# Performance work log

Hardware: AMD Instinct MI355X
Metric: run time of the kernel (lower is better)

The kernel has to match this reference:

```python
import jax, jax.numpy as jnp
import numpy as np
import math

B, S, HID = 4, 2048, 1024
H, D = 16, HID // 16


def setup_inputs() -> dict:
    key = jax.random.key(0)
    ks = jax.random.split(key, 6)
    scale = 0.02
    inp = {
        "hidden_states": jax.random.normal(ks[0], (B, S, HID), dtype=jnp.float32),
        "Wq": jax.random.normal(ks[1], (HID, HID), dtype=jnp.float32) * scale,
        "bq": jnp.zeros((HID,), dtype=jnp.float32),
        "Wk1": jax.random.normal(ks[2], (HID, HID), dtype=jnp.float32) * scale,
        "bk1": jnp.zeros((HID,), dtype=jnp.float32),
        "Wk2": jax.random.normal(ks[3], (HID, HID), dtype=jnp.float32) * scale,
        "bk2": jnp.zeros((HID,), dtype=jnp.float32),
        "Wv1": jax.random.normal(ks[4], (HID, HID), dtype=jnp.float32) * scale,
        "bv1": jnp.zeros((HID,), dtype=jnp.float32),
        "Wv2": jax.random.normal(ks[5], (HID, HID), dtype=jnp.float32) * scale,
        "bv2": jnp.zeros((HID,), dtype=jnp.float32),
    }
    return inp


def _heads(x):
    # [B, S, HID] -> [B, H, S, D]
    return x.reshape(B, S, H, D).transpose(0, 2, 1, 3)


def reference(hidden_states, Wq, bq, Wk1, bk1, Wk2, bk2, Wv1, bv1, Wv2, bv2):
    # nn.Linear uses y = x @ W^T + b
    q = _heads(hidden_states @ Wq.T + bq)
    k1 = _heads(hidden_states @ Wk1.T + bk1)
    k2 = _heads(hidden_states @ Wk2.T + bk2)
    v1 = _heads(hidden_states @ Wv1.T + bv1)
    v2 = _heads(hidden_states @ Wv2.T + bv2)

    inv_sqrt_d = 1.0 / math.sqrt(D)
    scores = jnp.einsum('bhqd,bhkd->bhqk', q, k1) * inv_sqrt_d  # [B,H,S,S]
    probs = jax.nn.softmax(scores, axis=-1)
    ctx = jnp.einsum('bhqk,bhkd->bhqd', probs, v1)              # [B,H,S,D]
    ctx = jnp.einsum('bhqd,bhkd->bhqk', ctx, k2)                # [B,H,S,S]
    ctx = jnp.einsum('bhqk,bhkd->bhqd', ctx, v2)                # [B,H,S,D]
    # [B,H,S,D] -> [B,S,HID]
    return ctx.transpose(0, 2, 1, 3).reshape(B, S, HID)
```

## Files before the change

### kernel.cpp

```cpp
#include <hip/hip_runtime.h>
#include <hip/hip_bf16.h>

#define HIDD 1024
#define BATCH 4
#define SEQ 2048
#define NHEAD 16
#define HD 64
#define NW 5
#define MROWS (BATCH*SEQ)
#define NCOLS (NW*HIDD)

typedef __attribute__((ext_vector_type(8))) short bf16x8;
typedef __attribute__((ext_vector_type(4))) float f32x4;
typedef __attribute__((ext_vector_type(16))) float f32x16;
typedef __attribute__((ext_vector_type(4))) unsigned int uint4v;

__device__ __forceinline__ unsigned short f2b(float f) {
    __hip_bfloat16 h = __float2bfloat16(f);
    return __builtin_bit_cast(unsigned short, h);
}
__device__ __forceinline__ float b2f(unsigned short u) {
    __hip_bfloat16 h = __builtin_bit_cast(__hip_bfloat16, u);
    return __bfloat162float(h);
}

#if __has_builtin(__builtin_amdgcn_exp2f)
#define EXP2(x) __builtin_amdgcn_exp2f(x)
#else
#define EXP2(x) exp2f(x)
#endif

typedef __attribute__((address_space(1))) const void gvoid;
typedef __attribute__((address_space(3))) void lvoid;
__device__ __forceinline__ void gload16(const void* src, void* dst) {
    __builtin_amdgcn_global_load_lds((gvoid*)src, (lvoid*)dst, 16, 0, 0);
}

__global__ void cvt_kernel(const float* __restrict__ X,
                           const float* __restrict__ W0, const float* __restrict__ W1,
                           const float* __restrict__ W2, const float* __restrict__ W3,
                           const float* __restrict__ W4,
                           unsigned short* __restrict__ Xb, unsigned short* __restrict__ Wb)
{
    const int XN = MROWS * HIDD / 4;
    const int WN = HIDD * HIDD / 4;
    int i = blockIdx.x * 256 + threadIdx.x;
    if (i >= XN + 5 * WN) return;
    const float* src; unsigned short* dst; int off;
    if (i < XN) { src = X; dst = Xb; off = i; }
    else {
        int j = i - XN; int w = j / WN; int r = j - w * WN;
        src = (w == 0 ? W0 : w == 1 ? W1 : w == 2 ? W2 : w == 3 ? W3 : W4);
        dst = Wb + (long)w * HIDD * HIDD; off = r;
    }
    float4 v = ((const float4*)src)[off];
    short4 o;
    o.x = (short)f2b(v.x); o.y = (short)f2b(v.y);
    o.z = (short)f2b(v.z); o.w = (short)f2b(v.w);
    ((short4*)dst)[off] = o;
}

__global__ __launch_bounds__(256) void gemm_proj(
    const unsigned short* __restrict__ Xb, const unsigned short* __restrict__ Wb,
    const float* __restrict__ pb0, const float* __restrict__ pb1, const float* __restrict__ pb2,
    const float* __restrict__ pb3, const float* __restrict__ pb4,
    unsigned short* __restrict__ C)
{
    __shared__ unsigned short As[2][128 * 32];
    __shared__ unsigned short Bs[2][128 * 32];
    int tid = threadIdx.x;
    int n = blockIdx.x;
    int xcd = n & 7, o = n >> 3;
    int bn = xcd * 5 + (o >> 6);
    int bm = o & 63;
    int lane = tid & 63, w = tid >> 6;
    int wr = w >> 1, wc = w & 1;
    int q = lane & 15, g = lane >> 4;

    f32x4 acc[4][4] = {};

    const unsigned short* Ag = Xb + (long)(bm * 128) * HIDD;
    const unsigned short* Bg = Wb + (long)(bn * 128) * HIDD;
    int srow = lane >> 2;
    int scol = ((lane & 3) ^ ((lane >> 3) & 3)) * 8;

    auto stage = [&](int kidx, int buf) {
        int k0 = (kidx & 31) * 32;
#pragma unroll
        for (int t = 0; t < 2; ++t) {
            int li = t * 4 + w;
            int row = li * 16 + srow;
            gload16(Ag + (long)row * HIDD + k0 + scol, (char*)As[buf] + li * 1024 + (lane << 4));
            gload16(Bg + (long)row * HIDD + k0 + scol, (char*)Bs[buf] + li * 1024 + (lane << 4));
        }
    };

    stage(0, 0);
    stage(1, 1);
    int csw = (q >> 1) & 3;

    for (int it = 0; it < 32; ++it) {
        int cur = it & 1;
        asm volatile("s_waitcnt vmcnt(4)" ::: "memory");
        asm volatile("s_barrier" ::: "memory");

        bf16x8 af[4], bfr[4];
#pragma unroll
        for (int mt = 0; mt < 4; mt++)
            af[mt]  = *(const bf16x8*)((const char*)As[cur] + (wr * 64 + mt * 16 + q) * 64 + ((g ^ csw) << 4));
#pragma unroll
        for (int nt = 0; nt < 4; nt++)
            bfr[nt] = *(const bf16x8*)((const char*)Bs[cur] + (wc * 64 + nt * 16 + q) * 64 + ((g ^ csw) << 4));

        asm volatile("s_waitcnt lgkmcnt(0)" ::: "memory");
        asm volatile("s_barrier" ::: "memory");
        stage(it + 2, cur);

#pragma unroll
        for (int mt = 0; mt < 4; mt++)
#pragma unroll
            for (int nt = 0; nt < 4; nt++)
                acc[mt][nt] = __builtin_amdgcn_mfma_f32_16x16x32_bf16(af[mt], bfr[nt], acc[mt][nt], 0, 0, 0);
    }
    int ncol0 = bn * 128 + wc * 64 + q;
    int wsel = (bn * 128) >> 10;
    const float* bp = (wsel == 0 ? pb0 : wsel == 1 ? pb1 : wsel == 2 ? pb2 : wsel == 3 ? pb3 : pb4);
#pragma unroll
    for (int nt = 0; nt < 4; nt++) {
        int ncol = ncol0 + nt * 16;
        float bv = bp[ncol & 1023];
#pragma unroll
        for (int mt = 0; mt < 4; mt++) {
            int row = bm * 128 + wr * 64 + mt * 16 + g * 4;
#pragma unroll
            for (int r = 0; r < 4; r++)
                C[(long)(row + r) * NCOLS + ncol] = f2b(acc[mt][nt][r] + bv);
        }
    }
}

#define QSCALE 0.180336880f
#define LDV 72
#define NT (SEQ / 64)

__global__ __launch_bounds__(256, 4) void flash1(
    const unsigned short* __restrict__ C, unsigned short* __restrict__ ctx)
{
    __shared__ unsigned short Ks[2][64 * 64];
    __shared__ unsigned short Vs[2][64 * LDV];
    __shared__ float Lbuf[4][32];
    int tid = threadIdx.x;
    int lane = tid & 63, w = tid >> 6;
    int q32 = lane & 31, hi = lane >> 5;
    int n = blockIdx.x;
    int qt = (n >> 3) & 15;
    int bh = (n & 7) * 8 + (n >> 7);
    int b = bh >> 4, h = bh & 15;
    long rowbase = (long)(b * SEQ) * NCOLS;
    int s0 = qt * 128;

    const unsigned short* Kg = C + rowbase + 1 * HIDD + h * 64;
    const unsigned short* Vg = C + rowbase + 3 * HIDD + h * 64;

    int krlo = lane >> 3;
    int kch  = (lane & 7) ^ krlo;
    int kp = tid & 31, dc = tid >> 5;
    int rsw = q32 & 7;

    bf16x8 qreg[4];
    {
        const unsigned short* Qp = C + rowbase + (long)(s0 + w * 32 + q32) * NCOLS + h * 64;
#pragma unroll
        for (int s = 0; s < 4; ++s) {
            bf16x8 v = *(const bf16x8*)(Qp + s * 16 + hi * 8);
#pragma unroll
            for (int j = 0; j < 8; j++)
                v[j] = (short)f2b(b2f((unsigned short)v[j]) * QSCALE);
            qreg[s] = v;
        }
    }

#pragma unroll
    for (int t = 0; t < 2; ++t) {
        int li = t * 4 + w;
        gload16(Kg + (long)(li * 8 + krlo) * NCOLS + kch * 8,
                (char*)Ks[0] + li * 1024 + (lane << 4));
    }
    {
        const unsigned short* vsrc = Vg + (long)(2 * kp) * NCOLS + dc * 8;
        bf16x8 v0 = *(const bf16x8*)vsrc;
        bf16x8 v1 = *(const bf16x8*)(vsrc + NCOLS);
        unsigned int* VsW = (unsigned int*)Vs[0];
#pragma unroll
        for (int j = 0; j < 8; j++) {
            unsigned int pk = ((unsigned int)(unsigned short)v0[j]) |
                              (((unsigned int)(unsigned short)v1[j]) << 16);
            VsW[(dc * 8 + j) * (LDV / 2) + kp] = pk;
        }
    }
    __syncthreads();

    f32x16 O0 = {}, O1 = {};
    float l_run = 0.f;

    auto body = [&](int kt, int cur, int nxt) {
        int ktn = (kt + 1) & (NT - 1);
#pragma unroll
        for (int t = 0; t < 2; ++t) {
            int li = t * 4 + w;
            gload16(Kg + (long)(ktn * 64 + li * 8 + krlo) * NCOLS + kch * 8,
                    (char*)Ks[nxt] + li * 1024 + (lane << 4));
        }
        const unsigned short* nsrc = Vg + (long)(ktn * 64 + 2 * kp) * NCOLS + dc * 8;
        bf16x8 nv0 = *(const bf16x8*)nsrc;
        bf16x8 nv1 = *(const bf16x8*)(nsrc + NCOLS);

        float lsum = 0.f;
        __builtin_amdgcn_s_setprio(1);
#pragma unroll
        for (int kb = 0; kb < 2; ++kb) {
            f32x16 st = {};
#pragma unroll
            for (int s = 0; s < 4; ++s) {
                bf16x8 kf = *(const bf16x8*)((const char*)Ks[cur] +
                             ((kb * 32 + q32) << 7) + (((2 * s + hi) ^ rsw) << 4));
                st = __builtin_amdgcn_mfma_f32_32x32x16_bf16(kf, qreg[s], st, 0, 0, 0);
            }
            float e[16];
#pragma unroll
            for (int r = 0; r < 16; ++r) e[r] = EXP2(st[r]);
            lsum += (((e[0]+e[1])+(e[2]+e[3])) + ((e[4]+e[5])+(e[6]+e[7])))
                  + (((e[8]+e[9])+(e[10]+e[11])) + ((e[12]+e[13])+(e[14]+e[15])));
            unsigned int Cw[8];
#pragma unroll
            for (int p = 0; p < 8; ++p)
                asm("v_cvt_pk_bf16_f32 %0, %1, %2" : "=v"(Cw[p]) : "v"(e[2*p]), "v"(e[2*p+1]));
#pragma unroll
            for (int t2 = 0; t2 < 2; ++t2) {
                unsigned int a0 = Cw[t2*4+0], a1 = Cw[t2*4+1];
                unsigned int a2 = Cw[t2*4+2], a3 = Cw[t2*4+3];
                asm("v_permlane32_swap_b32 %0, %1" : "+v"(a0), "+v"(a2));
                asm("v_permlane32_swap_b32 %0, %1" : "+v"(a1), "+v"(a3));
                uint4v aw; aw[0] = a0; aw[1] = a1; aw[2] = a2; aw[3] = a3;
                bf16x8 af = __builtin_bit_cast(bf16x8, aw);
                int t = kb * 2 + t2;
#pragma unroll
                for (int nt = 0; nt < 2; ++nt) {
                    bf16x8 vf = *(const bf16x8*)((const char*)Vs[cur] +
                                 (nt * 32 + q32) * (LDV * 2) + t * 32 + hi * 16);
                    if (nt == 0) O0 = __builtin_amdgcn_mfma_f32_32x32x16_bf16(af, vf, O0, 0, 0, 0);
                    else         O1 = __builtin_amdgcn_mfma_f32_32x32x16_bf16(af, vf, O1, 0, 0, 0);
                }
            }
        }
        __builtin_amdgcn_s_setprio(0);
        l_run += lsum;
        {
            unsigned int* VsWn = (unsigned int*)Vs[nxt];
#pragma unroll
            for (int j = 0; j < 8; ++j) {
                unsigned int pk = ((unsigned int)(unsigned short)nv0[j]) |
                                  (((unsigned int)(unsigned short)nv1[j]) << 16);
                VsWn[(dc * 8 + j) * (LDV / 2) + kp] = pk;
            }
        }
        __syncthreads();
    };

    for (int kt = 0; kt < NT; kt += 2) {
        body(kt, 0, 1);
        body(kt + 1, 1, 0);
    }

    l_run += __shfl_xor(l_run, 32);
    float linv = 1.f / l_run;
    Lbuf[w][q32] = linv;
    asm volatile("s_waitcnt lgkmcnt(0)" ::: "memory");
#pragma unroll
    for (int reg = 0; reg < 16; ++reg) {
        int row = (reg & 3) + 8 * (reg >> 2) + 4 * hi;
        float lr = Lbuf[w][row];
        unsigned short* dst = ctx + ((long)bh * SEQ + s0 + w * 32 + row) * 64 + q32;
        dst[0]  = f2b(O0[reg] * lr);
        dst[32] = f2b(O1[reg] * lr);
    }
}

#define LDT2 72
__global__ __launch_bounds__(256) void m_partial(
    const unsigned short* __restrict__ C, float* __restrict__ part)
{
    __shared__ unsigned short Kt[64 * LDT2];
    __shared__ unsigned short Vt[64 * LDT2];
    int tid = threadIdx.x;
    int lane = tid & 63, w = tid >> 6;
    int q32 = lane & 31, hi = lane >> 5;
    int sc = blockIdx.x;
    int bh = blockIdx.y; int b = bh >> 4, h = bh & 15;
    const unsigned short* K2 = C + (long)(b * SEQ) * NCOLS + 2 * HIDD + h * 64;
    const unsigned short* V2 = C + (long)(b * SEQ) * NCOLS + 4 * HIDD + h * 64;
    int kp = tid & 31, dc = tid >> 5;
    int d2h = w >> 1, d1h = w & 1;
    unsigned int* KtW = (unsigned int*)Kt;
    unsigned int* VtW = (unsigned int*)Vt;
    f32x16 acc = {};

    for (int tk = 0; tk < 4; ++tk) {
        int sbase = sc * 256 + tk * 64;
        if (tk) __syncthreads();
        const unsigned short* ks = K2 + (long)(sbase + 2 * kp) * NCOLS + dc * 8;
        bf16x8 k0 = *(const bf16x8*)ks, k1 = *(const bf16x8*)(ks + NCOLS);
        const unsigned short* vs = V2 + (long)(sbase + 2 * kp) * NCOLS + dc * 8;
        bf16x8 v0 = *(const bf16x8*)vs, v1 = *(const bf16x8*)(vs + NCOLS);
#pragma unroll
        for (int j = 0; j < 8; ++j) {
            KtW[(dc * 8 + j) * (LDT2 / 2) + kp] =
                (unsigned int)(unsigned short)k0[j] | ((unsigned int)(unsigned short)k1[j] << 16);
            VtW[(dc * 8 + j) * (LDT2 / 2) + kp] =
                (unsigned int)(unsigned short)v0[j] | ((unsigned int)(unsigned short)v1[j] << 16);
        }
        __syncthreads();
#pragma unroll
        for (int t = 0; t < 4; ++t) {
            bf16x8 afr = *(const bf16x8*)(Vt + (d2h * 32 + q32) * LDT2 + t * 16 + hi * 8);
            bf16x8 bfr = *(const bf16x8*)(Kt + (d1h * 32 + q32) * LDT2 + t * 16 + hi * 8);
            acc = __builtin_amdgcn_mfma_f32_32x32x16_bf16(afr, bfr, acc, 0, 0, 0);
        }
    }
    float* dst = part + ((long)(sc * 64 + bh) << 12);
#pragma unroll
    for (int reg = 0; reg < 16; ++reg) {
        int d2 = d2h * 32 + (reg & 3) + 8 * (reg >> 2) + 4 * hi;
        dst[d2 * 64 + d1h * 32 + q32] = acc[reg];
    }
}

__global__ void m_reduce(const float* __restrict__ part, float* __restrict__ MT)
{
    int i = blockIdx.x * 256 + threadIdx.x;
    if (i >= 64 * 4096) return;
    int bh = i >> 12, e = i & 4095;
    float s = 0.f;
#pragma unroll
    for (int sc = 0; sc < 8; sc++) s += part[((long)(sc * 64 + bh) << 12) + e];
    MT[i] = s;
}

#define LDF 72
__global__ __launch_bounds__(256) void final_out(
    const unsigned short* __restrict__ ctx, const float* __restrict__ MT,
    float* __restrict__ out)
{
    __shared__ unsigned short cs[64 * LDF];
    __shared__ float ms[64 * 65];
    int tid = threadIdx.x;
    int st0 = blockIdx.x * 4;
    int bh = blockIdx.y; int b = bh >> 4, h = bh & 15;
    {
        const float* Msrc = MT + ((long)bh << 12);
        for (int i = tid; i < 4096; i += 256) ms[(i >> 6) * 65 + (i & 63)] = Msrc[i];
    }
    int s = tid & 63, d2b = (tid >> 6) * 16;
    for (int ti = 0; ti < 4; ++ti) {
        int st = st0 + ti;
        if (ti) __syncthreads();
        {
            int i = tid >> 2, dcx = tid & 3;
            const unsigned short* src = ctx + ((long)bh * SEQ + st * 64 + i) * 64 + dcx * 16;
            *(int4*)(cs + i * LDF + dcx * 16)     = *(const int4*)src;
            *(int4*)(cs + i * LDF + dcx * 16 + 8) = *(const int4*)(src + 8);
        }
        __syncthreads();
        float acc[16] = {};
        for (int d1 = 0; d1 < 64; d1 += 8) {
            bf16x8 cv = *(const bf16x8*)(cs + s * LDF + d1);
#pragma unroll
            for (int dd = 0; dd < 8; dd++) {
                float c = b2f((unsigned short)cv[dd]);
#pragma unroll
                for (int j = 0; j < 16; j++)
                    acc[j] += c * ms[(d2b + j) * 65 + d1 + dd];
            }
        }
        float* dst = out + (long)(b * SEQ + st * 64 + s) * HIDD + h * 64 + d2b;
#pragma unroll
        for (int j = 0; j < 16; j++) dst[j] = acc[j];
    }
}

extern "C" void kernel_launch(void* const* d_in, const int* in_sizes, int n_in,
                              void* d_out, int out_size, void* d_ws, size_t ws_size,
                              hipStream_t stream)
{
    const float* X   = (const float*)d_in[0];
    const float* Wq  = (const float*)d_in[1];
    const float* bq  = (const float*)d_in[2];
    const float* Wk1 = (const float*)d_in[3];
    const float* bk1 = (const float*)d_in[4];
    const float* Wk2 = (const float*)d_in[5];
    const float* bk2 = (const float*)d_in[6];
    const float* Wv1 = (const float*)d_in[7];
    const float* bv1 = (const float*)d_in[8];
    const float* Wv2 = (const float*)d_in[9];
    const float* bv2 = (const float*)d_in[10];

    char* ws = (char*)d_ws;
    unsigned short* Xb  = (unsigned short*)(ws);
    unsigned short* Wb  = (unsigned short*)(ws + 16777216);
    unsigned short* C   = (unsigned short*)(ws + 27262976);
    unsigned short* ctx = (unsigned short*)(ws + 111149056);
    float* part         = (float*)(ws + 127926272);
    float* MT           = (float*)(ws + 136314880);
    float* out = (float*)d_out;

    cvt_kernel<<<dim3(13312), 256, 0, stream>>>(X, Wq, Wk1, Wk2, Wv1, Wv2, Xb, Wb);
    gemm_proj<<<dim3(2560), 256, 0, stream>>>(Xb, Wb, bq, bk1, bk2, bv1, bv2, C);
    flash1<<<dim3(1024), 256, 0, stream>>>(C, ctx);
    m_partial<<<dim3(8, 64), 256, 0, stream>>>(C, part);
    m_reduce<<<dim3(1024), 256, 0, stream>>>(part, MT);
    final_out<<<dim3(8, 64), 256, 0, stream>>>(ctx, MT, out);
}
```

Baseline: 291.7 us.

## Enlarge projection GEMM tiles to 256x256 with 8 waves and split-K pipeline

```diff
diff --git a/kernel.cpp b/kernel.cpp
--- a/kernel.cpp
+++ b/kernel.cpp
@@ -60,80 +60,103 @@
     ((short4*)dst)[off] = o;
 }
 
-__global__ __launch_bounds__(256) void gemm_proj(
+#define READ_A(buf, kh, mh) \
+    _Pragma("unroll") \
+    for (int mt = 0; mt < 4; ++mt) \
+        af[mt] = *(const bf16x8*)((const char*)As[buf][kh] + \
+                  (wr * 128 + (mh) * 64 + mt * 16 + q) * 64 + ((g ^ csw) << 4));
+#define READ_B(buf, kh) \
+    _Pragma("unroll") \
+    for (int nt = 0; nt < 4; ++nt) \
+        bfr[nt] = *(const bf16x8*)((const char*)Bs[buf][kh] + \
+                  (wc * 64 + nt * 16 + q) * 64 + ((g ^ csw) << 4));
+#define MFMA_Q(mh) \
+    asm volatile("s_waitcnt lgkmcnt(0)" ::: "memory"); \
+    __builtin_amdgcn_sched_barrier(0); \
+    __builtin_amdgcn_s_setprio(1); \
+    _Pragma("unroll") \
+    for (int mt = 0; mt < 4; ++mt) \
+    _Pragma("unroll") \
+    for (int nt = 0; nt < 4; ++nt) \
+        acc[(mh) * 4 + mt][nt] = __builtin_amdgcn_mfma_f32_16x16x32_bf16( \
+            af[mt], bfr[nt], acc[(mh) * 4 + mt][nt], 0, 0, 0); \
+    __builtin_amdgcn_s_setprio(0);
+
+__global__ __launch_bounds__(512, 2) void gemm_proj(
     const unsigned short* __restrict__ Xb, const unsigned short* __restrict__ Wb,
     const float* __restrict__ pb0, const float* __restrict__ pb1, const float* __restrict__ pb2,
     const float* __restrict__ pb3, const float* __restrict__ pb4,
     unsigned short* __restrict__ C)
 {
-    __shared__ unsigned short As[2][128 * 32];
-    __shared__ unsigned short Bs[2][128 * 32];
+    __shared__ __align__(16) unsigned short As[2][2][256 * 32];
+    __shared__ __align__(16) unsigned short Bs[2][2][256 * 32];
     int tid = threadIdx.x;
     int n = blockIdx.x;
     int xcd = n & 7, o = n >> 3;
-    int bn = xcd * 5 + (o >> 6);
-    int bm = o & 63;
+    int bm = xcd * 4 + (o & 3);
+    int bn = o >> 2;
     int lane = tid & 63, w = tid >> 6;
-    int wr = w >> 1, wc = w & 1;
+    int wr = w >> 2, wc = w & 3;
     int q = lane & 15, g = lane >> 4;
-
-    f32x4 acc[4][4] = {};
-
-    const unsigned short* Ag = Xb + (long)(bm * 128) * HIDD;
-    const unsigned short* Bg = Wb + (long)(bn * 128) * HIDD;
-    int srow = lane >> 2;
-    int scol = ((lane & 3) ^ ((lane >> 3) & 3)) * 8;
-
-    auto stage = [&](int kidx, int buf) {
-        int k0 = (kidx & 31) * 32;
-#pragma unroll
-        for (int t = 0; t < 2; ++t) {
-            int li = t * 4 + w;
-            int row = li * 16 + srow;
-            gload16(Ag + (long)row * HIDD + k0 + scol, (char*)As[buf] + li * 1024 + (lane << 4));
-            gload16(Bg + (long)row * HIDD + k0 + scol, (char*)Bs[buf] + li * 1024 + (lane << 4));
-        }
+    int csw = (q >> 1) & 3;
+
+    f32x4 acc[8][4] = {};
+
+    const unsigned short* Ag = Xb + (long)(bm * 256) * HIDD;
+    const unsigned short* Bg = Wb + (long)(bn * 256) * HIDD;
+    int srow = tid >> 2;
+    int scol = ((tid & 3) ^ ((tid >> 3) & 3)) * 8;
+
+    auto stage = [&](const unsigned short* G, unsigned short* slot, int kc) {
+#pragma unroll
+        for (int l = 0; l < 2; ++l)
+            gload16(G + (long)(l * 128 + srow) * HIDD + kc + scol,
+                    (char*)slot + (l * 512 + tid) * 16);
     };
 
-    stage(0, 0);
-    stage(1, 1);
-    int csw = (q >> 1) & 3;
-
-    for (int it = 0; it < 32; ++it) {
-        int cur = it & 1;
-        asm volatile("s_waitcnt vmcnt(4)" ::: "memory");
+    stage(Ag, As[0][0], 0);
+    stage(Bg, Bs[0][0], 0);
+    stage(Ag, As[0][1], 32);
+    stage(Bg, Bs[0][1], 32);
+    stage(Ag, As[1][0], 64);
+    stage(Bg, Bs[1][0], 64);
+
+    for (int t = 0; t < 16; ++t) {
+        int buf = t & 1;
+        int kc1 = ((t + 1) & 15) * 64;
+        int kc2 = ((t + 2) & 15) * 64;
+        bf16x8 af[4], bfr[4];
+        asm volatile("s_waitcnt vmcnt(8)" ::: "memory");
         asm volatile("s_barrier" ::: "memory");
-
-        bf16x8 af[4], bfr[4];
-#pragma unroll
-        for (int mt = 0; mt < 4; mt++)
-            af[mt]  = *(const bf16x8*)((const char*)As[cur] + (wr * 64 + mt * 16 + q) * 64 + ((g ^ csw) << 4));
-#pragma unroll
-        for (int nt = 0; nt < 4; nt++)
-            bfr[nt] = *(const bf16x8*)((const char*)Bs[cur] + (wc * 64 + nt * 16 + q) * 64 + ((g ^ csw) << 4));
-
-        asm volatile("s_waitcnt lgkmcnt(0)" ::: "memory");
+        READ_A(buf, 0, 0)
+        READ_B(buf, 0)
+        stage(Ag, As[buf ^ 1][1], kc1 + 32);
+        MFMA_Q(0)
+        READ_A(buf, 0, 1)
+        stage(Bg, Bs[buf ^ 1][1], kc1 + 32);
+        MFMA_Q(1)
+        asm volatile("s_waitcnt vmcnt(8)" ::: "memory");
         asm volatile("s_barrier" ::: "memory");
-        stage(it + 2, cur);
-
-#pragma unroll
-        for (int mt = 0; mt < 4; mt++)
-#pragma unroll
-            for (int nt = 0; nt < 4; nt++)
-                acc[mt][nt] = __builtin_amdgcn_mfma_f32_16x16x32_bf16(af[mt], bfr[nt], acc[mt][nt], 0, 0, 0);
-    }
-    int ncol0 = bn * 128 + wc * 64 + q;
-    int wsel = (bn * 128) >> 10;
-    const float* bp = (wsel == 0 ? pb0 : wsel == 1 ? pb1 : wsel == 2 ? pb2 : wsel == 3 ? pb3 : pb4);
-#pragma unroll
-    for (int nt = 0; nt < 4; nt++) {
+        READ_A(buf, 1, 0)
+        READ_B(buf, 1)
+        stage(Ag, As[buf][0], kc2);
+        MFMA_Q(0)
+        READ_A(buf, 1, 1)
+        stage(Bg, Bs[buf][0], kc2);
+        MFMA_Q(1)
+    }
+
+    int ncol0 = bn * 256 + wc * 64 + q;
+    const float* bp = (bn < 4 ? pb0 : bn < 8 ? pb1 : bn < 12 ? pb2 : bn < 16 ? pb3 : pb4);
+#pragma unroll
+    for (int nt = 0; nt < 4; ++nt) {
         int ncol = ncol0 + nt * 16;
         float bv = bp[ncol & 1023];
 #pragma unroll
-        for (int mt = 0; mt < 4; mt++) {
-            int row = bm * 128 + wr * 64 + mt * 16 + g * 4;
-#pragma unroll
-            for (int r = 0; r < 4; r++)
+        for (int mt = 0; mt < 8; ++mt) {
+            int row = bm * 256 + wr * 128 + mt * 16 + g * 4;
+#pragma unroll
+            for (int r = 0; r < 4; ++r)
                 C[(long)(row + r) * NCOLS + ncol] = f2b(acc[mt][nt][r] + bv);
         }
     }
@@ -414,7 +437,7 @@
     float* out = (float*)d_out;
 
     cvt_kernel<<<dim3(13312), 256, 0, stream>>>(X, Wq, Wk1, Wk2, Wv1, Wv2, Xb, Wb);
-    gemm_proj<<<dim3(2560), 256, 0, stream>>>(Xb, Wb, bq, bk1, bk2, bv1, bv2, C);
+    gemm_proj<<<dim3(640), 512, 0, stream>>>(Xb, Wb, bq, bk1, bk2, bv1, bv2, C);
     flash1<<<dim3(1024), 256, 0, stream>>>(C, ctx);
     m_partial<<<dim3(8, 64), 256, 0, stream>>>(C, part);
     m_reduce<<<dim3(1024), 256, 0, stream>>>(part, MT);
```

Result: faster. 279.5 us (-4.2%).
